# Kernel tuning notes

Hardware: AMD Instinct MI355X
Metric: run time of the kernel (lower is better)

## Reference

```python
import jax, jax.numpy as jnp
import numpy as np
from jax import lax

NOISE_STD = 0.0005
ALPHA = 0.1
B, S, I, H, O = 128, 2000, 8, 512, 2
NUM_EXC, NUM_INH = 384, 128


def setup_inputs() -> dict:
    key = jax.random.key(0)
    ks = jax.random.split(key, 6)
    return {
        "input": jax.random.normal(ks[0], (B, S, I), dtype=jnp.float32),
        "noise": jax.random.normal(ks[1], (B, S, H), dtype=jnp.float32),
        "wi": jax.random.normal(ks[2], (I, H), dtype=jnp.float32) / np.sqrt(I),
        # excitatory rows in [0, 0.5], inhibitory rows in [-0.5, 0] (Dale's law)
        "wrec_exc": jax.random.uniform(ks[3], (NUM_EXC, H), dtype=jnp.float32, minval=0.0, maxval=0.5),
        "wrec_inh": jax.random.uniform(ks[4], (NUM_INH, H), dtype=jnp.float32, minval=-0.5, maxval=0.0),
        "wout": jax.random.normal(ks[5], (H, O), dtype=jnp.float32) / np.sqrt(H),
        "h0": jnp.zeros((H,), dtype=jnp.float32),
    }


def reference(input, noise, wi, wrec_exc, wrec_inh, wout, h0):
    batch = input.shape[0]
    # wrec rows: [exc sources; inh sources]
    wrec = jnp.concatenate([wrec_exc, wrec_inh], axis=0)  # [H, H]
    r0 = jnp.tanh(h0)  # [H]
    out0 = jnp.broadcast_to(r0 @ wout, (batch, wout.shape[1]))  # output[:, 0]
    h_init = jnp.broadcast_to(h0, (batch, h0.shape[0]))  # [B, H]
    # precompute input projection for steps 0..S-2 (last step's input unused)
    xproj = jnp.einsum("bsi,ih->sbh", input[:, :-1], wi)  # [S-1, B, H]
    noise_t = jnp.transpose(noise[:, :-1], (1, 0, 2))  # [S-1, B, H]

    def step(h, inp):
        x_t, n_t = inp
        r = jnp.tanh(h)
        h_new = h + NOISE_STD * n_t + ALPHA * (-h + r @ wrec.T + x_t)
        return h_new, jnp.tanh(h_new) @ wout  # emit output[:, i+1]

    _, outs = lax.scan(step, h_init, (xproj, noise_t))  # outs: [S-1, B, O]
    output = jnp.concatenate([out0[None], outs], axis=0)  # [S, B, O]
    return jnp.transpose(output, (1, 0, 2))  # [B, S, O]
```

## Files before the change

kernel.cpp:

```cpp
#include <hip/hip_runtime.h>
#include <cmath>


constexpr int kS = 2000, kI = 8, kH = 512, kO = 2;
constexpr float kNoiseStd = 0.0005f, kAlpha = 0.1f;

constexpr int GROUPS = 8;
constexpr int NSPL   = 2;
constexpr int JS     = 256;
constexpr int NTHR   = 512;
constexpr int NBLK   = GROUPS * NSPL;
constexpr int RSLOT  = 8192;

typedef _Float16 half8  __attribute__((ext_vector_type(8)));
typedef float    floatx4 __attribute__((ext_vector_type(4)));
typedef unsigned uintx4  __attribute__((ext_vector_type(4)));

#define MFMA16(A, B, C) __builtin_amdgcn_mfma_f32_16x16x32_f16((A), (B), (C), 0, 0, 0)
#define PIN8(a) asm volatile("" : "+v"((a)[0]), "+v"((a)[1]), "+v"((a)[2]), "+v"((a)[3]), \
                                   "+v"((a)[4]), "+v"((a)[5]), "+v"((a)[6]), "+v"((a)[7]))

static __device__ __forceinline__ unsigned ld_flag(const unsigned* p) {
  return __hip_atomic_load(p, __ATOMIC_RELAXED, __HIP_MEMORY_SCOPE_AGENT);
}
static __device__ __forceinline__ void st_flag(unsigned* p, unsigned v) {
  __hip_atomic_store(p, v, __ATOMIC_RELAXED, __HIP_MEMORY_SCOPE_AGENT);
}

static __device__ __forceinline__ float fast_tanh(float x) {
  const float ax = __builtin_fabsf(x);
  const float e = __builtin_amdgcn_exp2f(2.8853900817779268f * ax);
  const float r = __builtin_amdgcn_rcpf(e + 1.0f);
  return __builtin_copysignf(__builtin_fmaf(-2.0f, r, 1.0f), x);
}

__global__ __launch_bounds__(NTHR, 1) void rnn_k(
    const float* __restrict__ inp,
    const float* __restrict__ noise,
    const float* __restrict__ wi,
    const float* __restrict__ wexc,
    const float* __restrict__ winh,
    const float* __restrict__ wout,
    const float* __restrict__ h0,
    float* __restrict__ out,
    _Float16* __restrict__ rbuf,
    unsigned* __restrict__ flags)
{
  const int bid = blockIdx.x;
  const int g = bid & 7;
  const int c = bid >> 3;
  const int tid = threadIdx.x;
  const int w = tid >> 6;
  const int lane = tid & 63;
  const int l15 = lane & 15;
  const int lhi = lane >> 4;

  const int j0 = c * JS + w * 32 + l15;
  const int j1 = j0 + 16;
  const int ktp = c * 8 + w;
  const int jsub0 = l15 >> 3, jsub1 = 2 + (l15 >> 3), vv = l15 & 7;

  __shared__ _Float16 ldsA[2][RSLOT];
  __shared__ half8 ws_wout[16][64];
  __shared__ float ldsIN[16][kI];

  half8 wfo0[8], wfo1[8], wfp0[8], wfp1[8];
  {
    const float* wr0 = (j0 < 384) ? (wexc + (size_t)j0 * kH) : (winh + (size_t)(j0 - 384) * kH);
    const float* wr1 = (j1 < 384) ? (wexc + (size_t)j1 * kH) : (winh + (size_t)(j1 - 384) * kH);
    const int ko = (c * 8) * 32 + lhi * 8;
    const int kp = ((c ^ 1) * 8) * 32 + lhi * 8;
#pragma unroll
    for (int t = 0; t < 8; ++t) {
      half8 a, b, d, e;
#pragma unroll
      for (int v = 0; v < 8; ++v) {
        a[v] = (_Float16)wr0[ko + t * 32 + v];
        b[v] = (_Float16)wr1[ko + t * 32 + v];
        d[v] = (_Float16)wr0[kp + t * 32 + v];
        e[v] = (_Float16)wr1[kp + t * 32 + v];
      }
      wfo0[t] = a; wfo1[t] = b; wfp0[t] = d; wfp1[t] = e;
    }
    PIN8(wfo0); PIN8(wfo1); PIN8(wfp0); PIN8(wfp1);
  }

  float wiv0[8], wiv1[8];
#pragma unroll
  for (int i = 0; i < 8; ++i) { wiv0[i] = wi[i * kH + j0]; wiv1[i] = wi[i * kH + j1]; }

  if (c == 0 && w < 4) {
#pragma unroll
    for (int t = 0; t < 4; ++t) {
      const int kt = w * 4 + t;
      const int k0 = kt * 32 + lhi * 8;
      half8 hv;
#pragma unroll
      for (int v = 0; v < 8; ++v)
        hv[v] = (l15 < kO) ? (_Float16)wout[(size_t)(k0 + v) * kO + l15] : (_Float16)0.f;
      ws_wout[kt][lane] = hv;
    }
  }

  float hq0[4], hq1[4];
  {
    const float h00 = h0[j0], h01 = h0[j1];
#pragma unroll
    for (int q = 0; q < 4; ++q) { hq0[q] = h00; hq1[q] = h01; }
    const _Float16 r00 = (_Float16)fast_tanh(h00);
    const _Float16 r01 = (_Float16)fast_tanh(h01);
#pragma unroll
    for (int q = 0; q < 4; ++q) {
      const int bb = lhi * 4 + q;
      ldsA[0][ktp * 512 + (bb + 16 * jsub0) * 8 + vv] = r00;
      ldsA[0][ktp * 512 + (bb + 16 * jsub1) * 8 + vv] = r01;
    }
    const uintx4 pub = *(const uintx4*)((const char*)&ldsA[0][0] + ktp * 1024 + lane * 16);
    char* dst = (char*)rbuf + (size_t)(0 * GROUPS + g) * (RSLOT * 2) + ktp * 1024 + lane * 16;
    asm volatile("global_store_dwordx4 %0, %1, off sc0 sc1" :: "v"(dst), "v"(pub) : "memory");
  }
  __syncthreads();
  if (tid == 0) st_flag(&flags[(0 * GROUPS + g) * NSPL + c], 1u);

  for (int s = 0; s < kS; ++s) {
    const int cur = s & 1;
    const bool lastS = (s == kS - 1);
    if (lastS && c != 0) break;

    if (c == 0 && w == 7 && s > 0) {
      floatx4 oa = {0,0,0,0}, ob = {0,0,0,0};
      const char* bprev = (const char*)&ldsA[cur ^ 1][0];
#pragma unroll
      for (int kt = 0; kt < 16; kt += 2) {
        const half8 f0 = *(const half8*)(bprev + kt * 1024 + lane * 16);
        const half8 f1 = *(const half8*)(bprev + (kt + 1) * 1024 + lane * 16);
        oa = MFMA16(f0, ws_wout[kt][lane], oa);
        ob = MFMA16(f1, ws_wout[kt + 1][lane], ob);
      }
      if (l15 < kO) {
#pragma unroll
        for (int q = 0; q < 4; ++q)
          out[((size_t)(g * 16 + lhi * 4 + q) * kS + (s - 1)) * kO + l15] = oa[q] + ob[q];
      }
    }

    float nz0[4], nz1[4];
    float inv = 0.f;
    if (!lastS) {
#pragma unroll
      for (int q = 0; q < 4; ++q) {
        const int b = g * 16 + lhi * 4 + q;
        nz0[q] = noise[((size_t)b * kS + s) * kH + j0];
        nz1[q] = noise[((size_t)b * kS + s) * kH + j1];
      }
      if (w == 2 || w == 3) {
        const int ii = tid - 128;
        inv = inp[((size_t)(g * 16 + (ii >> 3)) * kS + s) * kI + (ii & 7)];
      }
    }

    {
      const unsigned need = (unsigned)(s + 1);
      const unsigned* fp = &flags[(cur * GROUPS + g) * NSPL + (c ^ 1)];
      while (ld_flag(fp) < need) {}
      asm volatile("" ::: "memory");
    }

    uintx4 pv;
    {
      const char* src = (const char*)rbuf + (size_t)(cur * GROUPS + g) * (RSLOT * 2)
                        + (c ^ 1) * 8192 + tid * 16;
      asm volatile("global_load_dwordx4 %0, %1, off sc0 sc1" : "=&v"(pv) : "v"(src) : "memory");
    }

    floatx4 a00 = {0,0,0,0}, a01 = {0,0,0,0}, a10 = {0,0,0,0}, a11 = {0,0,0,0};
    const char* base = (const char*)&ldsA[cur][0];
    const char* baseO = base + c * 8192;
    const char* baseP = base + (c ^ 1) * 8192;
#pragma unroll
    for (int t = 0; t < 8; t += 2) {
      const half8 f0 = *(const half8*)(baseO + t * 1024 + lane * 16);
      const half8 f1 = *(const half8*)(baseO + (t + 1) * 1024 + lane * 16);
      a00 = MFMA16(f0, wfo0[t], a00);
      a10 = MFMA16(f0, wfo1[t], a10);
      a01 = MFMA16(f1, wfo0[t + 1], a01);
      a11 = MFMA16(f1, wfo1[t + 1], a11);
    }
    __builtin_amdgcn_sched_barrier(0);
    asm volatile("s_waitcnt vmcnt(0)" : "+v"(pv) :: "memory");
    *(uintx4*)((char*)&ldsA[cur][0] + (c ^ 1) * 8192 + tid * 16) = pv;
    if (!lastS && (w == 2 || w == 3)) {
      const int ii = tid - 128;
      ldsIN[ii >> 3][ii & 7] = inv;
    }
    __syncthreads();

#pragma unroll
    for (int t = 0; t < 8; t += 2) {
      const half8 f0 = *(const half8*)(baseP + t * 1024 + lane * 16);
      const half8 f1 = *(const half8*)(baseP + (t + 1) * 1024 + lane * 16);
      a00 = MFMA16(f0, wfp0[t], a00);
      a10 = MFMA16(f0, wfp1[t], a10);
      a01 = MFMA16(f1, wfp0[t + 1], a01);
      a11 = MFMA16(f1, wfp1[t + 1], a11);
    }

    if (!lastS) {
      _Float16* lA = &ldsA[cur ^ 1][0];
#pragma unroll
      for (int q = 0; q < 4; ++q) {
        const int bb = lhi * 4 + q;
        const floatx4 iv0 = *(const floatx4*)&ldsIN[bb][0];
        const floatx4 iv1 = *(const floatx4*)&ldsIN[bb][4];
        float x0 = 0.f, x1 = 0.f;
#pragma unroll
        for (int i = 0; i < 4; ++i) {
          x0 = fmaf(iv0[i], wiv0[i], x0); x0 = fmaf(iv1[i], wiv0[i + 4], x0);
          x1 = fmaf(iv0[i], wiv1[i], x1); x1 = fmaf(iv1[i], wiv1[i + 4], x1);
        }
        const float y0 = a00[q] + a01[q], y1 = a10[q] + a11[q];
        const float h0n = hq0[q] + kNoiseStd * nz0[q] + kAlpha * (-hq0[q] + y0 + x0);
        const float h1n = hq1[q] + kNoiseStd * nz1[q] + kAlpha * (-hq1[q] + y1 + x1);
        hq0[q] = h0n; hq1[q] = h1n;
        lA[ktp * 512 + (bb + 16 * jsub0) * 8 + vv] = (_Float16)fast_tanh(h0n);
        lA[ktp * 512 + (bb + 16 * jsub1) * 8 + vv] = (_Float16)fast_tanh(h1n);
      }
      const uintx4 pub = *(const uintx4*)((const char*)lA + ktp * 1024 + lane * 16);
      char* dst = (char*)rbuf + (size_t)((cur ^ 1) * GROUPS + g) * (RSLOT * 2)
                  + ktp * 1024 + lane * 16;
      asm volatile("global_store_dwordx4 %0, %1, off sc0 sc1" :: "v"(dst), "v"(pub) : "memory");
    }
    __syncthreads();
    if (!lastS && tid == 0)
      st_flag(&flags[((cur ^ 1) * GROUPS + g) * NSPL + c], (unsigned)(s + 2));
  }

  if (c == 0 && w == 7) {
    const char* bfin = (const char*)&ldsA[(kS - 1) & 1][0];
    floatx4 oa = {0,0,0,0}, ob = {0,0,0,0};
#pragma unroll
    for (int kt = 0; kt < 16; kt += 2) {
      const half8 f0 = *(const half8*)(bfin + kt * 1024 + lane * 16);
      const half8 f1 = *(const half8*)(bfin + (kt + 1) * 1024 + lane * 16);
      oa = MFMA16(f0, ws_wout[kt][lane], oa);
      ob = MFMA16(f1, ws_wout[kt + 1][lane], ob);
    }
    if (l15 < kO) {
#pragma unroll
      for (int q = 0; q < 4; ++q)
        out[((size_t)(g * 16 + lhi * 4 + q) * kS + (kS - 1)) * kO + l15] = oa[q] + ob[q];
    }
  }
}

extern "C" void kernel_launch(void* const* d_in, const int* in_sizes, int n_in,
                              void* d_out, int out_size, void* d_ws, size_t ws_size,
                              hipStream_t stream) {
  const float* inp   = (const float*)d_in[0];
  const float* noise = (const float*)d_in[1];
  const float* wi    = (const float*)d_in[2];
  const float* wexc  = (const float*)d_in[3];
  const float* winh  = (const float*)d_in[4];
  const float* wout  = (const float*)d_in[5];
  const float* h0    = (const float*)d_in[6];

  _Float16* rbuf = (_Float16*)d_ws;
  const size_t rbytes = (size_t)2 * GROUPS * RSLOT * sizeof(_Float16);
  unsigned* flags = (unsigned*)((char*)d_ws + rbytes);

  hipMemsetAsync(flags, 0, 2 * GROUPS * NSPL * sizeof(unsigned), stream);
  rnn_k<<<NBLK, NTHR, 0, stream>>>(inp, noise, wi, wexc, winh, wout, h0,
                                   (float*)d_out, rbuf, flags);
}
```

Before: 4.627 ms.

## Replace flag-based inter-block sync with stamped data packets polled inline

Removes the separate per-block flag counters and the spin-wait on them. Each thread now publishes its 16-byte tanh slice split across two 16-byte stores, with the step number embedded in the upper bits of each store. Consumers poll their own packet until both stamps match. This drops the store→syncthreads→flag-store→flag-poll→load round trip in favour of a single poll-and-read, at the cost of doubling the exchange traffic and relying on each 16-byte store being visible atomically.

```diff
diff --git a/kernel.cpp b/kernel.cpp
--- a/kernel.cpp
+++ b/kernel.cpp
@@ -10,7 +10,9 @@
 constexpr int JS     = 256;
 constexpr int NTHR   = 512;
 constexpr int NBLK   = GROUPS * NSPL;
-constexpr int RSLOT  = 8192;
+
+constexpr int SCHUNK = 2048;
+constexpr int SSLOT  = 16 * SCHUNK;
 
 typedef _Float16 half8  __attribute__((ext_vector_type(8)));
 typedef float    floatx4 __attribute__((ext_vector_type(4)));
@@ -19,19 +21,20 @@
 #define MFMA16(A, B, C) __builtin_amdgcn_mfma_f32_16x16x32_f16((A), (B), (C), 0, 0, 0)
 #define PIN8(a) asm volatile("" : "+v"((a)[0]), "+v"((a)[1]), "+v"((a)[2]), "+v"((a)[3]), \
                                    "+v"((a)[4]), "+v"((a)[5]), "+v"((a)[6]), "+v"((a)[7]))
-
-static __device__ __forceinline__ unsigned ld_flag(const unsigned* p) {
-  return __hip_atomic_load(p, __ATOMIC_RELAXED, __HIP_MEMORY_SCOPE_AGENT);
-}
-static __device__ __forceinline__ void st_flag(unsigned* p, unsigned v) {
-  __hip_atomic_store(p, v, __ATOMIC_RELAXED, __HIP_MEMORY_SCOPE_AGENT);
-}
 
 static __device__ __forceinline__ float fast_tanh(float x) {
   const float ax = __builtin_fabsf(x);
   const float e = __builtin_amdgcn_exp2f(2.8853900817779268f * ax);
   const float r = __builtin_amdgcn_rcpf(e + 1.0f);
   return __builtin_copysignf(__builtin_fmaf(-2.0f, r, 1.0f), x);
+}
+
+static __device__ __forceinline__ void stamp_pack(const uintx4 d, unsigned stamp,
+                                                  uintx4& sa, uintx4& sb) {
+  sa[0] = d[0]; sa[1] = d[1]; sa[2] = d[2];
+  sa[3] = (stamp << 16) | (d[3] & 0xffffu);
+  sb[0] = (stamp << 16) | (d[3] >> 16);
+  sb[1] = stamp; sb[2] = stamp; sb[3] = stamp;
 }
 
 __global__ __launch_bounds__(NTHR, 1) void rnn_k(
@@ -43,8 +46,7 @@
     const float* __restrict__ wout,
     const float* __restrict__ h0,
     float* __restrict__ out,
-    _Float16* __restrict__ rbuf,
-    unsigned* __restrict__ flags)
+    char* __restrict__ sbuf)
 {
   const int bid = blockIdx.x;
   const int g = bid & 7;
@@ -60,7 +62,7 @@
   const int ktp = c * 8 + w;
   const int jsub0 = l15 >> 3, jsub1 = 2 + (l15 >> 3), vv = l15 & 7;
 
-  __shared__ _Float16 ldsA[2][RSLOT];
+  __shared__ _Float16 ldsA[2][8192];
   __shared__ half8 ws_wout[16][64];
   __shared__ float ldsIN[16][kI];
 
@@ -116,11 +118,13 @@
       ldsA[0][ktp * 512 + (bb + 16 * jsub1) * 8 + vv] = r01;
     }
     const uintx4 pub = *(const uintx4*)((const char*)&ldsA[0][0] + ktp * 1024 + lane * 16);
-    char* dst = (char*)rbuf + (size_t)(0 * GROUPS + g) * (RSLOT * 2) + ktp * 1024 + lane * 16;
-    asm volatile("global_store_dwordx4 %0, %1, off sc0 sc1" :: "v"(dst), "v"(pub) : "memory");
+    uintx4 sa, sb;
+    stamp_pack(pub, 1u, sa, sb);
+    char* dst = sbuf + (size_t)(0 * GROUPS + g) * SSLOT + ktp * SCHUNK + lane * 32;
+    asm volatile("global_store_dwordx4 %0, %1, off sc0 sc1" :: "v"(dst), "v"(sa) : "memory");
+    asm volatile("global_store_dwordx4 %0, %1, off offset:16 sc0 sc1" :: "v"(dst), "v"(sb) : "memory");
   }
   __syncthreads();
-  if (tid == 0) st_flag(&flags[(0 * GROUPS + g) * NSPL + c], 1u);
 
   for (int s = 0; s < kS; ++s) {
     const int cur = s & 1;
@@ -157,20 +161,6 @@
         const int ii = tid - 128;
         inv = inp[((size_t)(g * 16 + (ii >> 3)) * kS + s) * kI + (ii & 7)];
       }
-    }
-
-    {
-      const unsigned need = (unsigned)(s + 1);
-      const unsigned* fp = &flags[(cur * GROUPS + g) * NSPL + (c ^ 1)];
-      while (ld_flag(fp) < need) {}
-      asm volatile("" ::: "memory");
-    }
-
-    uintx4 pv;
-    {
-      const char* src = (const char*)rbuf + (size_t)(cur * GROUPS + g) * (RSLOT * 2)
-                        + (c ^ 1) * 8192 + tid * 16;
-      asm volatile("global_load_dwordx4 %0, %1, off sc0 sc1" : "=&v"(pv) : "v"(src) : "memory");
     }
 
     floatx4 a00 = {0,0,0,0}, a01 = {0,0,0,0}, a10 = {0,0,0,0}, a11 = {0,0,0,0};
@@ -186,9 +176,23 @@
       a01 = MFMA16(f1, wfo0[t + 1], a01);
       a11 = MFMA16(f1, wfo1[t + 1], a11);
     }
-    __builtin_amdgcn_sched_barrier(0);
-    asm volatile("s_waitcnt vmcnt(0)" : "+v"(pv) :: "memory");
-    *(uintx4*)((char*)&ldsA[cur][0] + (c ^ 1) * 8192 + tid * 16) = pv;
+
+    {
+      const char* src = sbuf + (size_t)(cur * GROUPS + g) * SSLOT
+                        + ((c ^ 1) * 8 + w) * SCHUNK + lane * 32;
+      const unsigned want = (unsigned)(s + 1);
+      uintx4 ua, ub;
+      do {
+        asm volatile("global_load_dwordx4 %0, %2, off sc0 sc1\n\t"
+                     "global_load_dwordx4 %1, %2, off offset:16 sc0 sc1\n\t"
+                     "s_waitcnt vmcnt(0)"
+                     : "=&v"(ua), "=&v"(ub) : "v"(src) : "memory");
+      } while ((ua[3] >> 16) != want || (ub[0] >> 16) != want);
+      uintx4 pv;
+      pv[0] = ua[0]; pv[1] = ua[1]; pv[2] = ua[2];
+      pv[3] = (ub[0] << 16) | (ua[3] & 0xffffu);
+      *(uintx4*)((char*)&ldsA[cur][0] + (c ^ 1) * 8192 + tid * 16) = pv;
+    }
     if (!lastS && (w == 2 || w == 3)) {
       const int ii = tid - 128;
       ldsIN[ii >> 3][ii & 7] = inv;
@@ -226,13 +230,13 @@
         lA[ktp * 512 + (bb + 16 * jsub1) * 8 + vv] = (_Float16)fast_tanh(h1n);
       }
       const uintx4 pub = *(const uintx4*)((const char*)lA + ktp * 1024 + lane * 16);
-      char* dst = (char*)rbuf + (size_t)((cur ^ 1) * GROUPS + g) * (RSLOT * 2)
-                  + ktp * 1024 + lane * 16;
-      asm volatile("global_store_dwordx4 %0, %1, off sc0 sc1" :: "v"(dst), "v"(pub) : "memory");
+      uintx4 sa, sb;
+      stamp_pack(pub, (unsigned)(s + 2), sa, sb);
+      char* dst = sbuf + (size_t)((cur ^ 1) * GROUPS + g) * SSLOT + ktp * SCHUNK + lane * 32;
+      asm volatile("global_store_dwordx4 %0, %1, off sc0 sc1" :: "v"(dst), "v"(sa) : "memory");
+      asm volatile("global_store_dwordx4 %0, %1, off offset:16 sc0 sc1" :: "v"(dst), "v"(sb) : "memory");
     }
     __syncthreads();
-    if (!lastS && tid == 0)
-      st_flag(&flags[((cur ^ 1) * GROUPS + g) * NSPL + c], (unsigned)(s + 2));
   }
 
   if (c == 0 && w == 7) {
@@ -264,11 +268,8 @@
   const float* wout  = (const float*)d_in[5];
   const float* h0    = (const float*)d_in[6];
 
-  _Float16* rbuf = (_Float16*)d_ws;
-  const size_t rbytes = (size_t)2 * GROUPS * RSLOT * sizeof(_Float16);
-  unsigned* flags = (unsigned*)((char*)d_ws + rbytes);
-
-  hipMemsetAsync(flags, 0, 2 * GROUPS * NSPL * sizeof(unsigned), stream);
+  const size_t sbytes = (size_t)2 * GROUPS * SSLOT;
+  hipMemsetAsync(d_ws, 0, sbytes, stream);
   rnn_k<<<NBLK, NTHR, 0, stream>>>(inp, noise, wi, wexc, winh, wout, h0,
-                                   (float*)d_out, rbuf, flags);
-}
+                                   (float*)d_out, (char*)d_ws);
+}
```

Measured after the change: 5.829 ms. 1.26x slower.
